# Performance work log

Measured on AMD Instinct MI355X. Metric: run time of the kernel, lower is better.

The kernel has to match this reference:

```python
import jax, jax.numpy as jnp
import numpy as np

B, E, C, M, H = 4, 8, 512, 1024, 4096

def setup_inputs() -> dict:
    key = jax.random.key(0)
    k1, k2, k3, k4, k5 = jax.random.split(key, 5)
    s = 1.0 / np.sqrt(M)
    return {
        "x": jax.random.normal(k1, (B, E, C, M), dtype=jnp.float32),
        "fc1_weight": jax.random.normal(k2, (E, H, M), dtype=jnp.float32) * s,
        "fc1_bias": jax.random.normal(k3, (E, 1, H), dtype=jnp.float32) * 0.02,
        "fc2_weight": jax.random.normal(k4, (E, H, M), dtype=jnp.float32) * (1.0 / np.sqrt(H)),
        "fc2_bias": jax.random.normal(k5, (E, 1, M), dtype=jnp.float32) * 0.02,
    }

def reference(x, fc1_weight, fc1_bias, fc2_weight, fc2_bias):
    # x: [B, E, C, M] -> [E, B*C, M]
    b, e, c, m = x.shape
    xe = jnp.transpose(x, (1, 0, 2, 3)).reshape(e, b * c, m)
    # fc1: [E,T,M] @ [E,M,H] (fp32 grouped GEMM with bias)
    h = jnp.einsum('etm,ehm->eth', xe.astype(jnp.float32), fc1_weight.astype(jnp.float32)) + fc1_bias.astype(jnp.float32)
    h = jax.nn.relu(h)
    # fc2: [E,T,H] @ [E,H,M] + bias (dropout is identity)
    o = jnp.einsum('eth,ehm->etm', h, fc2_weight) + fc2_bias
    o = o.reshape(e, b, c, m)
    return jnp.transpose(o, (1, 0, 2, 3))
```

## Files before the change

kernel.cpp:

```cpp
#include <hip/hip_runtime.h>
#include <hip/hip_bf16.h>

typedef __bf16 bf16x8 __attribute__((ext_vector_type(8)));
typedef __bf16 bf16x4 __attribute__((ext_vector_type(4)));
typedef float  f32x4  __attribute__((ext_vector_type(4)));

constexpr int Ee = 8, Cc = 512, Mm = 1024, Hh = 4096, Tt = 2048;

__device__ __forceinline__ void async16(void* lds, const void* g) {
  __builtin_amdgcn_global_load_lds(
      (const __attribute__((address_space(1))) void*)g,
      (__attribute__((address_space(3))) void*)lds, 16, 0, 0);
}

#define FENCE() asm volatile("" ::: "memory")
#define BARRIER() do { FENCE(); __builtin_amdgcn_s_barrier(); FENCE(); } while (0)

__device__ __forceinline__ int xcd_swz(int id, int n) {
  const int q = n >> 3, r = n & 7;
  const int x = id & 7, k = id >> 3;
  return (x < r ? x * (q + 1) : r * (q + 1) + (x - r) * q) + k;
}

__device__ __forceinline__ void gemm256(
    const __bf16* __restrict__ aT, const __bf16* __restrict__ bT, const int K,
    __bf16 (*Ab)[2][128][64], __bf16 (*Bb)[2][128][64],
    f32x4 (&acc)[8][4]) {
  const int tid = threadIdx.x;
  const int lane = tid & 63, wid = tid >> 6;
  const int wr = wid >> 2, wcn = wid & 3;
  const int l8 = lane >> 3;
  const int colSwzE = (((lane & 7) ^ l8) << 3);
  const int NT = K >> 6;

  int pblk[2];
  pblk[0] = (lane >> 4) ^ (lane & 7);
  pblk[1] = (4 + (lane >> 4)) ^ (lane & 7);

  bf16x8 aF[8][2];
  bf16x8 bFa[2][2];
  bf16x8 bFb[2][2];

  auto STAGE = [&](int s, int u) {
    if (s >= NT) return;
    const int d = s & 1;
    if (u < 2) {
      const __bf16* src = aT + (size_t)(u * 128 + wid * 16 + l8) * K + s * 64 + colSwzE;
#pragma unroll
      for (int i = 0; i < 2; ++i)
        async16(&Ab[d][u][wid * 16 + i * 8][0], src + (size_t)(i * 8) * K);
    } else {
      const __bf16* src = bT + (size_t)((u - 2) * 128 + wid * 16 + l8) * K + s * 64 + colSwzE;
#pragma unroll
      for (int i = 0; i < 2; ++i)
        async16(&Bb[d][u - 2][wid * 16 + i * 8][0], src + (size_t)(i * 8) * K);
    }
  };

  STAGE(0, 0); STAGE(0, 1); STAGE(0, 2); STAGE(0, 3);
  STAGE(1, 0); STAGE(1, 1);
  asm volatile("s_waitcnt vmcnt(4)" ::: "memory");
  BARRIER();

  for (int t = 0; t < NT; ++t) {
    const int d = t & 1;
    const char* pa = (const char*)&Ab[d][wr][0][0];
    const char* pb = (const char*)&Bb[d][wcn >> 1][0][0];
    const int brow = (wcn & 1) * 64;

#pragma unroll
    for (int mi = 0; mi < 4; ++mi)
#pragma unroll
      for (int kh = 0; kh < 2; ++kh)
        aF[mi][kh] = *(const bf16x8*)(pa + (mi * 16 + (lane & 15)) * 128 + pblk[kh] * 16);
#pragma unroll
    for (int ni = 0; ni < 2; ++ni)
#pragma unroll
      for (int kh = 0; kh < 2; ++kh)
        bFa[ni][kh] = *(const bf16x8*)(pb + (brow + ni * 16 + (lane & 15)) * 128 + pblk[kh] * 16);
    STAGE(t + 1, 2);
    asm volatile("s_waitcnt lgkmcnt(8)" ::: "memory");
    BARRIER();
    asm volatile("s_waitcnt lgkmcnt(0)" ::: "memory");
    __builtin_amdgcn_s_setprio(1);
#pragma unroll
    for (int mi = 0; mi < 4; ++mi)
#pragma unroll
      for (int ni = 0; ni < 2; ++ni)
#pragma unroll
        for (int kh = 0; kh < 2; ++kh)
          acc[mi][ni] = __builtin_amdgcn_mfma_f32_16x16x32_bf16(bFa[ni][kh], aF[mi][kh], acc[mi][ni], 0, 0, 0);
    __builtin_amdgcn_s_setprio(0);
    BARRIER();

#pragma unroll
    for (int mi = 0; mi < 4; ++mi)
#pragma unroll
      for (int kh = 0; kh < 2; ++kh)
        aF[4 + mi][kh] = *(const bf16x8*)(pa + ((4 + mi) * 16 + (lane & 15)) * 128 + pblk[kh] * 16);
    STAGE(t + 1, 3);
    BARRIER();
    asm volatile("s_waitcnt lgkmcnt(0)" ::: "memory");
    __builtin_amdgcn_s_setprio(1);
#pragma unroll
    for (int mi = 0; mi < 4; ++mi)
#pragma unroll
      for (int ni = 0; ni < 2; ++ni)
#pragma unroll
        for (int kh = 0; kh < 2; ++kh)
          acc[4 + mi][ni] = __builtin_amdgcn_mfma_f32_16x16x32_bf16(bFa[ni][kh], aF[4 + mi][kh], acc[4 + mi][ni], 0, 0, 0);
    __builtin_amdgcn_s_setprio(0);
    BARRIER();

#pragma unroll
    for (int ni = 0; ni < 2; ++ni)
#pragma unroll
      for (int kh = 0; kh < 2; ++kh)
        bFb[ni][kh] = *(const bf16x8*)(pb + (brow + (2 + ni) * 16 + (lane & 15)) * 128 + pblk[kh] * 16);
    STAGE(t + 2, 0);
    BARRIER();
    asm volatile("s_waitcnt lgkmcnt(0)" ::: "memory");
    __builtin_amdgcn_s_setprio(1);
#pragma unroll
    for (int mi = 0; mi < 4; ++mi)
#pragma unroll
      for (int ni = 0; ni < 2; ++ni)
#pragma unroll
        for (int kh = 0; kh < 2; ++kh)
          acc[4 + mi][2 + ni] = __builtin_amdgcn_mfma_f32_16x16x32_bf16(bFb[ni][kh], aF[4 + mi][kh], acc[4 + mi][2 + ni], 0, 0, 0);
    __builtin_amdgcn_s_setprio(0);
    BARRIER();

    STAGE(t + 2, 1);
    __builtin_amdgcn_s_setprio(1);
#pragma unroll
    for (int mi = 0; mi < 4; ++mi)
#pragma unroll
      for (int ni = 0; ni < 2; ++ni)
#pragma unroll
        for (int kh = 0; kh < 2; ++kh)
          acc[mi][2 + ni] = __builtin_amdgcn_mfma_f32_16x16x32_bf16(bFb[ni][kh], aF[mi][kh], acc[mi][2 + ni], 0, 0, 0);
    __builtin_amdgcn_s_setprio(0);
    if (t < NT - 2) { asm volatile("s_waitcnt vmcnt(4)" ::: "memory"); }
    else            { asm volatile("s_waitcnt vmcnt(0)" ::: "memory"); }
    BARRIER();
  }
}

__global__ __launch_bounds__(512, 2) void fc1g_kernel(
    const __bf16* __restrict__ xb, int eOffA,
    const __bf16* __restrict__ w1b, int eOffB,
    const float* __restrict__ b1, __bf16* __restrict__ hb,
    int e0, int t_base, int tcap, int nbT) {
  __shared__ __bf16 Ab[2][2][128][64];
  __shared__ __bf16 Bb[2][2][128][64];
  const int nbN = Hh / 256;
  const int id = xcd_swz(blockIdx.x, gridDim.x);
  const int z = id / (nbN * nbT);
  const int rm = id % (nbN * nbT);
  const int tblk = (rm / nbN) * 256, nblk = (rm % nbN) * 256;
  const int lane = threadIdx.x & 63, wid = threadIdx.x >> 6;
  const int wr = wid >> 2, wcn = wid & 3;

  const __bf16* aT = xb + ((size_t)(eOffA + z) * Tt + t_base + tblk) * Mm;
  const __bf16* bT = w1b + ((size_t)(eOffB + z) * Hh + nblk) * Mm;

  f32x4 acc[8][4];
#pragma unroll
  for (int i = 0; i < 8; ++i)
#pragma unroll
    for (int j = 0; j < 4; ++j) acc[i][j] = (f32x4){0.f, 0.f, 0.f, 0.f};

  gemm256(aT, bT, Mm, Ab, Bb, acc);

  const float* bias = b1 + (size_t)(e0 + z) * Hh;
#pragma unroll
  for (int ni = 0; ni < 4; ++ni) {
    const int n0 = nblk + wcn * 64 + ni * 16 + ((lane >> 4) << 2);
    const f32x4 b4 = *(const f32x4*)(bias + n0);
#pragma unroll
    for (int mi = 0; mi < 8; ++mi) {
      const int trow = tblk + wr * 128 + mi * 16 + (lane & 15);
      f32x4 v = acc[mi][ni];
      bf16x4 o;
#pragma unroll
      for (int rr = 0; rr < 4; ++rr) {
        float f = v[rr] + b4[rr];
        o[rr] = (__bf16)(f > 0.f ? f : 0.f);
      }
      *(bf16x4*)(hb + ((size_t)z * tcap + trow) * Hh + n0) = o;
    }
  }
}

__global__ __launch_bounds__(512, 2) void fc2g_kernel(
    const __bf16* __restrict__ hb, int tcap,
    const __bf16* __restrict__ w2t, int eOffB,
    const float* __restrict__ b2, float* __restrict__ out,
    int e0, int t_base, int nbT) {
  __shared__ __bf16 Ab[2][2][128][64];
  __shared__ __bf16 Bb[2][2][128][64];
  const int nbN = Mm / 256;
  const int id = xcd_swz(blockIdx.x, gridDim.x);
  const int z = id / (nbN * nbT);
  const int rm = id % (nbN * nbT);
  const int tblk = (rm / nbN) * 256, nblk = (rm % nbN) * 256;
  const int lane = threadIdx.x & 63, wid = threadIdx.x >> 6;
  const int wr = wid >> 2, wcn = wid & 3;
  const int e = e0 + z;

  const __bf16* aT = hb + ((size_t)z * tcap + tblk) * Hh;
  const __bf16* bT = w2t + ((size_t)(eOffB + z) * Mm + nblk) * Hh;

  f32x4 acc[8][4];
#pragma unroll
  for (int i = 0; i < 8; ++i)
#pragma unroll
    for (int j = 0; j < 4; ++j) acc[i][j] = (f32x4){0.f, 0.f, 0.f, 0.f};

  gemm256(aT, bT, Hh, Ab, Bb, acc);

  const float* bias = b2 + (size_t)e * Mm;
#pragma unroll
  for (int ni = 0; ni < 4; ++ni) {
    const int m0 = nblk + wcn * 64 + ni * 16 + ((lane >> 4) << 2);
    const f32x4 b4 = *(const f32x4*)(bias + m0);
#pragma unroll
    for (int mi = 0; mi < 8; ++mi) {
      const int t = t_base + tblk + wr * 128 + mi * 16 + (lane & 15);
      const int bb = t >> 9, cc = t & 511;
      f32x4 v = acc[mi][ni];
#pragma unroll
      for (int rr = 0; rr < 4; ++rr) v[rr] += b4[rr];
      *(f32x4*)(out + ((((size_t)bb * Ee + e) * Cc + cc) << 10) + m0) = v;
    }
  }
}

__global__ __launch_bounds__(256) void cvt_x_kernel(
    const float* __restrict__ x, __bf16* __restrict__ xb, int e0) {
  size_t idx8 = (size_t)blockIdx.x * 256 + threadIdx.x;
  int m8 = (int)(idx8 & 127);
  int t = (int)((idx8 >> 7) & 2047);
  int z = (int)(idx8 >> 18);
  int b = t >> 9, c = t & 511, e = e0 + z;
  const float* src = x + ((((size_t)b * Ee + e) * Cc + c) << 10) + (m8 << 3);
  f32x4 v0 = *(const f32x4*)src;
  f32x4 v1 = *(const f32x4*)(src + 4);
  bf16x8 o;
  o[0] = (__bf16)v0[0]; o[1] = (__bf16)v0[1]; o[2] = (__bf16)v0[2]; o[3] = (__bf16)v0[3];
  o[4] = (__bf16)v1[0]; o[5] = (__bf16)v1[1]; o[6] = (__bf16)v1[2]; o[7] = (__bf16)v1[3];
  *(bf16x8*)(xb + (idx8 << 3)) = o;
}

__global__ __launch_bounds__(256) void cvt_lin_kernel(
    const float* __restrict__ in, __bf16* __restrict__ outb) {
  size_t i8 = (size_t)blockIdx.x * 256 + threadIdx.x;
  const float* src = in + (i8 << 3);
  f32x4 v0 = *(const f32x4*)src;
  f32x4 v1 = *(const f32x4*)(src + 4);
  bf16x8 o;
  o[0] = (__bf16)v0[0]; o[1] = (__bf16)v0[1]; o[2] = (__bf16)v0[2]; o[3] = (__bf16)v0[3];
  o[4] = (__bf16)v1[0]; o[5] = (__bf16)v1[1]; o[6] = (__bf16)v1[2]; o[7] = (__bf16)v1[3];
  *(bf16x8*)(outb + (i8 << 3)) = o;
}

__global__ __launch_bounds__(256) void tr_w2_kernel(
    const float* __restrict__ w2, __bf16* __restrict__ w2t, int e0) {
  __shared__ __bf16 tile[64][68];
  const int z = blockIdx.z, e = e0 + z;
  const int m0 = blockIdx.x * 64, h0 = blockIdx.y * 64;
  const int tid = threadIdx.x;
  const int cg = tid & 15, rg = tid >> 4;
#pragma unroll
  for (int p = 0; p < 4; ++p) {
    int hl = rg + p * 16;
    f32x4 v = *(const f32x4*)(w2 + (((size_t)e * Hh + h0 + hl) << 10) + m0 + (cg << 2));
#pragma unroll
    for (int i = 0; i < 4; ++i) tile[(cg << 2) + i][hl] = (__bf16)v[i];
  }
  __syncthreads();
#pragma unroll
  for (int p = 0; p < 4; ++p) {
    int ml = rg + p * 16;
    uint2 pk = *(const uint2*)(&tile[ml][cg << 2]);
    *(uint2*)(w2t + ((size_t)z * Mm + m0 + ml) * Hh + h0 + (cg << 2)) = pk;
  }
}

extern "C" void kernel_launch(void* const* d_in, const int* in_sizes, int n_in,
                              void* d_out, int out_size, void* d_ws, size_t ws_size,
                              hipStream_t stream) {
  const float* x  = (const float*)d_in[0];
  const float* w1 = (const float*)d_in[1];
  const float* b1 = (const float*)d_in[2];
  const float* w2 = (const float*)d_in[3];
  const float* b2 = (const float*)d_in[4];
  float* out = (float*)d_out;

  const size_t xbS = (size_t)Tt * Mm * 2;
  const size_t w1S = (size_t)Hh * Mm * 2;
  const size_t w2S = (size_t)Mm * Hh * 2;
  const size_t hbS = (size_t)Tt * Hh * 2;
  char* ws = (char*)d_ws;

  if (ws_size >= Ee * (xbS + w1S + w2S + hbS)) {
    __bf16* xb  = (__bf16*)ws;
    __bf16* w1b = (__bf16*)(ws + Ee * xbS);
    __bf16* w2t = (__bf16*)(ws + Ee * (xbS + w1S));
    __bf16* hb  = (__bf16*)(ws + Ee * (xbS + w1S + w2S));
    cvt_x_kernel<<<Ee * 1024, 256, 0, stream>>>(x, xb, 0);
    cvt_lin_kernel<<<Ee * 2048, 256, 0, stream>>>(w1, w1b);
    tr_w2_kernel<<<dim3(Mm / 64, Hh / 64, Ee), 256, 0, stream>>>(w2, w2t, 0);
    fc1g_kernel<<<(Hh / 256) * (Tt / 256) * Ee, 512, 0, stream>>>(xb, 0, w1b, 0, b1, hb, 0, 0, Tt, Tt / 256);
    fc2g_kernel<<<(Mm / 256) * (Tt / 256) * Ee, 512, 0, stream>>>(hb, Tt, w2t, 0, b2, out, 0, 0, Tt / 256);
  } else if (ws_size >= Ee * (xbS + w1S + w2S) + hbS) {
    __bf16* xb  = (__bf16*)ws;
    __bf16* w1b = (__bf16*)(ws + Ee * xbS);
    __bf16* w2t = (__bf16*)(ws + Ee * (xbS + w1S));
    __bf16* hb  = (__bf16*)(ws + Ee * (xbS + w1S + w2S));
    int Gh = (int)((ws_size - Ee * (xbS + w1S + w2S)) / hbS);
    if (Gh > Ee) Gh = Ee;
    cvt_x_kernel<<<Ee * 1024, 256, 0, stream>>>(x, xb, 0);
    cvt_lin_kernel<<<Ee * 2048, 256, 0, stream>>>(w1, w1b);
    tr_w2_kernel<<<dim3(Mm / 64, Hh / 64, Ee), 256, 0, stream>>>(w2, w2t, 0);
    for (int e0 = 0; e0 < Ee; e0 += Gh) {
      int g = (Ee - e0) < Gh ? (Ee - e0) : Gh;
      fc1g_kernel<<<(Hh / 256) * (Tt / 256) * g, 512, 0, stream>>>(xb, e0, w1b, e0, b1, hb, e0, 0, Tt, Tt / 256);
      fc2g_kernel<<<(Mm / 256) * (Tt / 256) * g, 512, 0, stream>>>(hb, Tt, w2t, e0, b2, out, e0, 0, Tt / 256);
    }
  } else if (ws_size >= xbS + w1S + w2S + hbS) {
    int G = (int)(ws_size / (xbS + w1S + w2S + hbS));
    if (G > Ee) G = Ee;
    __bf16* xb  = (__bf16*)ws;
    __bf16* w1b = (__bf16*)(ws + (size_t)G * xbS);
    __bf16* w2t = (__bf16*)(ws + (size_t)G * (xbS + w1S));
    __bf16* hb  = (__bf16*)(ws + (size_t)G * (xbS + w1S + w2S));
    for (int e0 = 0; e0 < Ee; e0 += G) {
      int g = (Ee - e0) < G ? (Ee - e0) : G;
      cvt_x_kernel<<<g * 1024, 256, 0, stream>>>(x, xb, e0);
      cvt_lin_kernel<<<g * 2048, 256, 0, stream>>>(w1 + (size_t)e0 * Hh * Mm, w1b);
      tr_w2_kernel<<<dim3(Mm / 64, Hh / 64, g), 256, 0, stream>>>(w2, w2t, e0);
      fc1g_kernel<<<(Hh / 256) * (Tt / 256) * g, 512, 0, stream>>>(xb, 0, w1b, 0, b1, hb, e0, 0, Tt, Tt / 256);
      fc2g_kernel<<<(Mm / 256) * (Tt / 256) * g, 512, 0, stream>>>(hb, Tt, w2t, 0, b2, out, e0, 0, Tt / 256);
    }
  } else {
    __bf16* xb  = (__bf16*)ws;
    __bf16* w1b = (__bf16*)(ws + xbS);
    __bf16* w2t = (__bf16*)(ws + xbS + w1S);
    __bf16* hb  = (__bf16*)(ws + xbS + w1S + w2S);
    size_t rem = ws_size > (xbS + w1S + w2S) ? ws_size - (xbS + w1S + w2S) : 0;
    int Tc = (int)(rem / ((size_t)Hh * 2)) & ~255;
    if (Tc > Tt) Tc = Tt;
    if (Tc < 256) Tc = 256;
    for (int e0 = 0; e0 < Ee; ++e0) {
      cvt_x_kernel<<<1024, 256, 0, stream>>>(x, xb, e0);
      cvt_lin_kernel<<<2048, 256, 0, stream>>>(w1 + (size_t)e0 * Hh * Mm, w1b);
      tr_w2_kernel<<<dim3(Mm / 64, Hh / 64, 1), 256, 0, stream>>>(w2, w2t, e0);
      for (int t0 = 0; t0 < Tt; t0 += Tc) {
        int tc = (Tt - t0) < Tc ? (Tt - t0) : Tc;
        fc1g_kernel<<<(Hh / 256) * (tc / 256), 512, 0, stream>>>(xb, 0, w1b, 0, b1, hb, e0, t0, Tc, tc / 256);
        fc2g_kernel<<<(Mm / 256) * (tc / 256), 512, 0, stream>>>(hb, Tc, w2t, 0, b2, out, e0, t0, tc / 256);
      }
    }
  }
}
```

Measured before the change: 445.4 us.

## Triple-buffer A tiles, drop intra-iteration barriers, launch experts in groups

The shared GEMM mainloop now triple-buffers the A operand and double-buffers B, with separate staging helpers. This removes most of the per-phase barriers and lgkmcnt waits, leaving a single barrier per K step, so LDS reads and MFMA work can overlap global-to-LDS loads more freely. The full-workspace path also now launches fc1/fc2 in two groups of four experts, which shrinks the live intermediate buffer and may improve cache locality. The larger A buffer raises per-block LDS to about 160 KB, which likely prevents the two blocks per CU asked for by the launch bounds.

Result: slower. 557.3 us (+25.1%).

```diff
diff --git a/kernel.cpp b/kernel.cpp
--- a/kernel.cpp
+++ b/kernel.cpp
@@ -24,7 +24,8 @@
 
 __device__ __forceinline__ void gemm256(
     const __bf16* __restrict__ aT, const __bf16* __restrict__ bT, const int K,
-    __bf16 (*Ab)[2][128][64], __bf16 (*Bb)[2][128][64],
+    __bf16 (*Ab)[2][128][64],
+    __bf16 (*Bb)[2][128][64],
     f32x4 (&acc)[8][4]) {
   const int tid = threadIdx.x;
   const int lane = tid & 63, wid = tid >> 6;
@@ -41,32 +42,41 @@
   bf16x8 bFa[2][2];
   bf16x8 bFb[2][2];
 
-  auto STAGE = [&](int s, int u) {
+  auto STAGE_A = [&](int s, int slot) {
     if (s >= NT) return;
-    const int d = s & 1;
-    if (u < 2) {
+#pragma unroll
+    for (int u = 0; u < 2; ++u) {
       const __bf16* src = aT + (size_t)(u * 128 + wid * 16 + l8) * K + s * 64 + colSwzE;
 #pragma unroll
       for (int i = 0; i < 2; ++i)
-        async16(&Ab[d][u][wid * 16 + i * 8][0], src + (size_t)(i * 8) * K);
-    } else {
-      const __bf16* src = bT + (size_t)((u - 2) * 128 + wid * 16 + l8) * K + s * 64 + colSwzE;
+        async16(&Ab[slot][u][wid * 16 + i * 8][0], src + (size_t)(i * 8) * K);
+    }
+  };
+  auto STAGE_B = [&](int s) {
+    if (s >= NT) return;
+    const int slot = s & 1;
+#pragma unroll
+    for (int u = 0; u < 2; ++u) {
+      const __bf16* src = bT + (size_t)(u * 128 + wid * 16 + l8) * K + s * 64 + colSwzE;
 #pragma unroll
       for (int i = 0; i < 2; ++i)
-        async16(&Bb[d][u - 2][wid * 16 + i * 8][0], src + (size_t)(i * 8) * K);
+        async16(&Bb[slot][u][wid * 16 + i * 8][0], src + (size_t)(i * 8) * K);
     }
   };
 
-  STAGE(0, 0); STAGE(0, 1); STAGE(0, 2); STAGE(0, 3);
-  STAGE(1, 0); STAGE(1, 1);
+  STAGE_A(0, 0);
+  STAGE_B(0);
+  STAGE_A(1, 1);
   asm volatile("s_waitcnt vmcnt(4)" ::: "memory");
   BARRIER();
 
+  int rdA = 0, stA = 2;
   for (int t = 0; t < NT; ++t) {
-    const int d = t & 1;
-    const char* pa = (const char*)&Ab[d][wr][0][0];
-    const char* pb = (const char*)&Bb[d][wcn >> 1][0][0];
+    const char* pa = (const char*)&Ab[rdA][wr][0][0];
+    const char* pb = (const char*)&Bb[t & 1][wcn >> 1][0][0];
     const int brow = (wcn & 1) * 64;
+
+    STAGE_B(t + 1);
 
 #pragma unroll
     for (int mi = 0; mi < 4; ++mi)
@@ -78,10 +88,9 @@
 #pragma unroll
       for (int kh = 0; kh < 2; ++kh)
         bFa[ni][kh] = *(const bf16x8*)(pb + (brow + ni * 16 + (lane & 15)) * 128 + pblk[kh] * 16);
-    STAGE(t + 1, 2);
-    asm volatile("s_waitcnt lgkmcnt(8)" ::: "memory");
-    BARRIER();
-    asm volatile("s_waitcnt lgkmcnt(0)" ::: "memory");
+
+    STAGE_A(t + 2, stA);
+
     __builtin_amdgcn_s_setprio(1);
 #pragma unroll
     for (int mi = 0; mi < 4; ++mi)
@@ -91,16 +100,13 @@
         for (int kh = 0; kh < 2; ++kh)
           acc[mi][ni] = __builtin_amdgcn_mfma_f32_16x16x32_bf16(bFa[ni][kh], aF[mi][kh], acc[mi][ni], 0, 0, 0);
     __builtin_amdgcn_s_setprio(0);
-    BARRIER();
 
 #pragma unroll
     for (int mi = 0; mi < 4; ++mi)
 #pragma unroll
       for (int kh = 0; kh < 2; ++kh)
         aF[4 + mi][kh] = *(const bf16x8*)(pa + ((4 + mi) * 16 + (lane & 15)) * 128 + pblk[kh] * 16);
-    STAGE(t + 1, 3);
-    BARRIER();
-    asm volatile("s_waitcnt lgkmcnt(0)" ::: "memory");
+
     __builtin_amdgcn_s_setprio(1);
 #pragma unroll
     for (int mi = 0; mi < 4; ++mi)
@@ -110,16 +116,13 @@
         for (int kh = 0; kh < 2; ++kh)
           acc[4 + mi][ni] = __builtin_amdgcn_mfma_f32_16x16x32_bf16(bFa[ni][kh], aF[4 + mi][kh], acc[4 + mi][ni], 0, 0, 0);
     __builtin_amdgcn_s_setprio(0);
-    BARRIER();
 
 #pragma unroll
     for (int ni = 0; ni < 2; ++ni)
 #pragma unroll
       for (int kh = 0; kh < 2; ++kh)
         bFb[ni][kh] = *(const bf16x8*)(pb + (brow + (2 + ni) * 16 + (lane & 15)) * 128 + pblk[kh] * 16);
-    STAGE(t + 2, 0);
-    BARRIER();
-    asm volatile("s_waitcnt lgkmcnt(0)" ::: "memory");
+
     __builtin_amdgcn_s_setprio(1);
 #pragma unroll
     for (int mi = 0; mi < 4; ++mi)
@@ -128,11 +131,6 @@
 #pragma unroll
         for (int kh = 0; kh < 2; ++kh)
           acc[4 + mi][2 + ni] = __builtin_amdgcn_mfma_f32_16x16x32_bf16(bFb[ni][kh], aF[4 + mi][kh], acc[4 + mi][2 + ni], 0, 0, 0);
-    __builtin_amdgcn_s_setprio(0);
-    BARRIER();
-
-    STAGE(t + 2, 1);
-    __builtin_amdgcn_s_setprio(1);
 #pragma unroll
     for (int mi = 0; mi < 4; ++mi)
 #pragma unroll
@@ -141,9 +139,12 @@
         for (int kh = 0; kh < 2; ++kh)
           acc[mi][2 + ni] = __builtin_amdgcn_mfma_f32_16x16x32_bf16(bFb[ni][kh], aF[mi][kh], acc[mi][2 + ni], 0, 0, 0);
     __builtin_amdgcn_s_setprio(0);
+
     if (t < NT - 2) { asm volatile("s_waitcnt vmcnt(4)" ::: "memory"); }
     else            { asm volatile("s_waitcnt vmcnt(0)" ::: "memory"); }
     BARRIER();
+    rdA = (rdA == 2) ? 0 : rdA + 1;
+    stA = (stA == 2) ? 0 : stA + 1;
   }
 }
 
@@ -152,7 +153,7 @@
     const __bf16* __restrict__ w1b, int eOffB,
     const float* __restrict__ b1, __bf16* __restrict__ hb,
     int e0, int t_base, int tcap, int nbT) {
-  __shared__ __bf16 Ab[2][2][128][64];
+  __shared__ __bf16 Ab[3][2][128][64];
   __shared__ __bf16 Bb[2][2][128][64];
   const int nbN = Hh / 256;
   const int id = xcd_swz(blockIdx.x, gridDim.x);
@@ -198,7 +199,7 @@
     const __bf16* __restrict__ w2t, int eOffB,
     const float* __restrict__ b2, float* __restrict__ out,
     int e0, int t_base, int nbT) {
-  __shared__ __bf16 Ab[2][2][128][64];
+  __shared__ __bf16 Ab[3][2][128][64];
   __shared__ __bf16 Bb[2][2][128][64];
   const int nbN = Mm / 256;
   const int id = xcd_swz(blockIdx.x, gridDim.x);
@@ -304,7 +305,7 @@
   const size_t hbS = (size_t)Tt * Hh * 2;
   char* ws = (char*)d_ws;
 
-  if (ws_size >= Ee * (xbS + w1S + w2S + hbS)) {
+  if (ws_size >= Ee * (xbS + w1S + w2S) + 4 * hbS) {
     __bf16* xb  = (__bf16*)ws;
     __bf16* w1b = (__bf16*)(ws + Ee * xbS);
     __bf16* w2t = (__bf16*)(ws + Ee * (xbS + w1S));
@@ -312,8 +313,10 @@
     cvt_x_kernel<<<Ee * 1024, 256, 0, stream>>>(x, xb, 0);
     cvt_lin_kernel<<<Ee * 2048, 256, 0, stream>>>(w1, w1b);
     tr_w2_kernel<<<dim3(Mm / 64, Hh / 64, Ee), 256, 0, stream>>>(w2, w2t, 0);
-    fc1g_kernel<<<(Hh / 256) * (Tt / 256) * Ee, 512, 0, stream>>>(xb, 0, w1b, 0, b1, hb, 0, 0, Tt, Tt / 256);
-    fc2g_kernel<<<(Mm / 256) * (Tt / 256) * Ee, 512, 0, stream>>>(hb, Tt, w2t, 0, b2, out, 0, 0, Tt / 256);
+    for (int e0 = 0; e0 < Ee; e0 += 4) {
+      fc1g_kernel<<<(Hh / 256) * (Tt / 256) * 4, 512, 0, stream>>>(xb, e0, w1b, e0, b1, hb, e0, 0, Tt, Tt / 256);
+      fc2g_kernel<<<(Mm / 256) * (Tt / 256) * 4, 512, 0, stream>>>(hb, Tt, w2t, e0, b2, out, e0, 0, Tt / 256);
+    }
   } else if (ws_size >= Ee * (xbS + w1S + w2S) + hbS) {
     __bf16* xb  = (__bf16*)ws;
     __bf16* w1b = (__bf16*)(ws + Ee * xbS);
```
